# Kernel optimization log

Measured on AMD Instinct MI355X. Metric: run time of the kernel, lower is better.

The kernel has to match this reference:

```python
import jax, jax.numpy as jnp
import numpy as np

N_NODES = 100000
N_EDGES = 1200000
D_IN, D_HID, D_OUT = 64, 64, 16


def setup_inputs() -> dict:
    key = jax.random.key(0)
    ks = jax.random.split(key, 8)
    x = jax.random.normal(ks[0], (N_NODES, D_IN), dtype=jnp.float32)
    edge_index = jax.random.randint(ks[1], (2, N_EDGES), 0, N_NODES, dtype=jnp.int64)
    edge_weight = jax.random.uniform(ks[2], (N_EDGES,), dtype=jnp.float32)
    s1 = 1.0 / np.sqrt(D_IN)
    s2 = 1.0 / np.sqrt(D_HID)
    W1l = jax.random.normal(ks[3], (D_IN, D_HID), dtype=jnp.float32) * s1
    W1r = jax.random.normal(ks[4], (D_IN, D_HID), dtype=jnp.float32) * s1
    b1 = jnp.zeros((D_HID,), dtype=jnp.float32)
    W2l = jax.random.normal(ks[5], (D_HID, D_OUT), dtype=jnp.float32) * s2
    W2r = jax.random.normal(ks[6], (D_HID, D_OUT), dtype=jnp.float32) * s2
    b2 = jnp.zeros((D_OUT,), dtype=jnp.float32)
    return {"x": x, "edge_index": edge_index, "edge_weight": edge_weight,
            "W1l": W1l, "b1": b1, "W1r": W1r, "W2l": W2l, "b2": b2, "W2r": W2r}


def _sage_conv(x, src, dst, ew, Wl, bl, Wr):
    # message: x_j * w_e, mean-aggregated by in-degree count at dst (PyG SAGEConv aggr='mean')
    msg = x[src] * ew[:, None]                                  # [E, D]
    agg = jax.ops.segment_sum(msg, dst, num_segments=x.shape[0])
    cnt = jax.ops.segment_sum(jnp.ones_like(ew), dst, num_segments=x.shape[0])
    agg = agg / jnp.maximum(cnt, 1.0)[:, None]
    return agg @ Wl + bl + x @ Wr                               # lin_l(agg) + lin_r(x)


def reference(x, edge_index, edge_weight, W1l, b1, W1r, W2l, b2, W2r):
    # eval mode: dropout is identity
    src, dst = edge_index[0], edge_index[1]
    h = jax.nn.relu(_sage_conv(x, src, dst, edge_weight, W1l, b1, W1r))
    out = _sage_conv(h, src, dst, edge_weight, W2l, b2, W2r)
    return out
```

## Files before the change

kernel.cpp:

```cpp
#include <hip/hip_runtime.h>

#define N_NODES 100000
#define N_EDGES 1200000
#define NB_SCAN ((N_NODES + 1023) / 1024)

__global__ __launch_bounds__(256) void k_hist(const int* __restrict__ ei,
                                              int* __restrict__ deg) {
    int e = blockIdx.x * 256 + threadIdx.x;
    if (e < N_EDGES) atomicAdd(&deg[ei[N_EDGES + e]], 1);
}

__global__ __launch_bounds__(256) void k_scanA(const int* __restrict__ deg,
                                               int* __restrict__ bsum) {
    const int b = blockIdx.x, t = threadIdx.x;
    const int base = b * 1024 + t * 4;
    int s = 0;
    #pragma unroll
    for (int i = 0; i < 4; ++i) {
        int idx = base + i;
        if (idx < N_NODES) s += deg[idx];
    }
    #pragma unroll
    for (int off = 1; off < 64; off <<= 1) s += __shfl_xor(s, off);
    __shared__ int part[4];
    if ((t & 63) == 0) part[t >> 6] = s;
    __syncthreads();
    if (t == 0) bsum[b] = part[0] + part[1] + part[2] + part[3];
}

__global__ void k_scanB(const int* __restrict__ bsum, int* __restrict__ boff) {
    if (threadIdx.x == 0) {
        int acc = 0;
        for (int i = 0; i < NB_SCAN; ++i) { boff[i] = acc; acc += bsum[i]; }
    }
}

__global__ __launch_bounds__(256) void k_scanC(const int* __restrict__ deg,
                                               const int* __restrict__ boff,
                                               int* __restrict__ row_ptr) {
    __shared__ int tot[256];
    const int b = blockIdx.x, t = threadIdx.x;
    const int base = b * 1024 + t * 4;
    int d[4]; int s = 0;
    #pragma unroll
    for (int i = 0; i < 4; ++i) {
        int idx = base + i;
        d[i] = (idx < N_NODES) ? deg[idx] : 0;
        s += d[i];
    }
    tot[t] = s;
    __syncthreads();
    for (int off = 1; off < 256; off <<= 1) {
        int v = (t >= off) ? tot[t - off] : 0;
        __syncthreads();
        tot[t] += v;
        __syncthreads();
    }
    int run = boff[b] + tot[t] - s;
    #pragma unroll
    for (int i = 0; i < 4; ++i) {
        int idx = base + i;
        if (idx < N_NODES) { row_ptr[idx] = run; run += d[i]; }
    }
    if (b == 0 && t == 0) row_ptr[N_NODES] = N_EDGES;
}

__global__ __launch_bounds__(256) void k_fill(const int* __restrict__ ei,
                                              const float* __restrict__ ew,
                                              int* __restrict__ cursor,
                                              uint2* __restrict__ csr) {
    int e = blockIdx.x * 256 + threadIdx.x;
    if (e < N_EDGES) {
        int src = ei[e];
        int dst = ei[N_EDGES + e];
        int pos = atomicAdd(&cursor[dst], 1);
        csr[pos] = make_uint2((unsigned)src, __float_as_uint(ew[e]));
    }
}

__global__ __launch_bounds__(512, 2) void k_l1(const float* __restrict__ x,
                                               const int* __restrict__ row_ptr,
                                               const uint2* __restrict__ csr,
                                               const float* __restrict__ W1l,
                                               const float* __restrict__ b1,
                                               const float* __restrict__ W1r,
                                               const float* __restrict__ W2l,
                                               const float* __restrict__ W2r,
                                               float* __restrict__ z2,
                                               float* __restrict__ hw2r) {
    __shared__ float w1l[64 * 64];
    __shared__ float w1r[64 * 64];
    __shared__ float w2l[64 * 17];
    __shared__ float w2r[64 * 17];
    for (int i = threadIdx.x; i < 64 * 64; i += 512) { w1l[i] = W1l[i]; w1r[i] = W1r[i]; }
    for (int i = threadIdx.x; i < 64 * 16; i += 512) {
        int k = i >> 4, j = i & 15;
        w2l[k * 17 + j] = W2l[i];
        w2r[k * 17 + j] = W2r[i];
    }
    __syncthreads();
    const int lane = threadIdx.x & 63;
    const int wid  = blockIdx.x * 8 + (threadIdx.x >> 6);
    const int nw   = gridDim.x * 8;
    const int j = lane & 15, g = lane >> 4;
    const float b1v = b1[lane];
    for (int n = wid; n < N_NODES; n += nw) {
        const int r0 = row_ptr[n], r1 = row_ptr[n + 1];
        const int deg = r1 - r0;
        float acc0 = 0.f, acc1 = 0.f, acc2 = 0.f, acc3 = 0.f;
        for (int base = r0; base < r1; base += 64) {
            const int m = r1 - base < 64 ? r1 - base : 64;
            uint2 sw = make_uint2(0u, 0u);
            if (lane < m) sw = csr[base + lane];
            const int sv = (int)sw.x;
            const int wv = (int)sw.y;
            int it = 0;
            for (; it + 4 <= m; it += 4) {
                int s0 = __builtin_amdgcn_readlane(sv, it);
                int s1 = __builtin_amdgcn_readlane(sv, it + 1);
                int s2 = __builtin_amdgcn_readlane(sv, it + 2);
                int s3 = __builtin_amdgcn_readlane(sv, it + 3);
                float w0 = __int_as_float(__builtin_amdgcn_readlane(wv, it));
                float w1 = __int_as_float(__builtin_amdgcn_readlane(wv, it + 1));
                float w2 = __int_as_float(__builtin_amdgcn_readlane(wv, it + 2));
                float w3 = __int_as_float(__builtin_amdgcn_readlane(wv, it + 3));
                float v0 = x[(size_t)s0 * 64 + lane];
                float v1 = x[(size_t)s1 * 64 + lane];
                float v2 = x[(size_t)s2 * 64 + lane];
                float v3 = x[(size_t)s3 * 64 + lane];
                acc0 = fmaf(v0, w0, acc0);
                acc1 = fmaf(v1, w1, acc1);
                acc2 = fmaf(v2, w2, acc2);
                acc3 = fmaf(v3, w3, acc3);
            }
            for (; it < m; ++it) {
                int   s = __builtin_amdgcn_readlane(sv, it);
                float w = __int_as_float(__builtin_amdgcn_readlane(wv, it));
                acc0 = fmaf(x[(size_t)s * 64 + lane], w, acc0);
            }
        }
        const float acc = (acc0 + acc1) + (acc2 + acc3);
        const float inv = 1.f / (float)(deg > 0 ? deg : 1);
        const float av  = acc * inv;
        const float xr  = x[(size_t)n * 64 + lane];
        float hacc = b1v;
        #pragma unroll
        for (int k = 0; k < 64; ++k) {
            float ak = __shfl(av, k);
            float xk = __shfl(xr, k);
            hacc = fmaf(ak, w1l[k * 64 + lane], hacc);
            hacc = fmaf(xk, w1r[k * 64 + lane], hacc);
        }
        const float hval = hacc > 0.f ? hacc : 0.f;

        float azv = 0.f, arv = 0.f;
        #pragma unroll
        for (int i = 0; i < 16; ++i) {
            int   k  = g * 16 + i;
            float hk = __shfl(hval, k);
            azv = fmaf(hk, w2l[k * 17 + j], azv);
            arv = fmaf(hk, w2r[k * 17 + j], arv);
        }
        azv += __shfl_xor(azv, 16); azv += __shfl_xor(azv, 32);
        arv += __shfl_xor(arv, 16); arv += __shfl_xor(arv, 32);
        if (g == 0) {
            z2[(size_t)n * 16 + j]   = azv;
            hw2r[(size_t)n * 16 + j] = arv;
        }
    }
}

__global__ __launch_bounds__(256) void k_l2(const float* __restrict__ z2,
                                            const int* __restrict__ row_ptr,
                                            const uint2* __restrict__ csr,
                                            const float* __restrict__ b2,
                                            const float* __restrict__ hw2r,
                                            float* __restrict__ out) {
    const int lane = threadIdx.x & 63;
    const int wid  = blockIdx.x * 4 + (threadIdx.x >> 6);
    const int nw   = gridDim.x * 4;
    const int j = lane & 15, g = lane >> 4;
    for (int n = wid; n < N_NODES; n += nw) {
        const int r0 = row_ptr[n], r1 = row_ptr[n + 1];
        const int deg = r1 - r0;
        float a = 0.f;
        int i = r0 + g;
        for (; i + 4 < r1; i += 8) {
            uint2 e0 = csr[i];
            uint2 e1 = csr[i + 4];
            float z0 = z2[(size_t)e0.x * 16 + j];
            float z1 = z2[(size_t)e1.x * 16 + j];
            a = fmaf(z0, __uint_as_float(e0.y), a);
            a = fmaf(z1, __uint_as_float(e1.y), a);
        }
        if (i < r1) {
            uint2 e0 = csr[i];
            a = fmaf(z2[(size_t)e0.x * 16 + j], __uint_as_float(e0.y), a);
        }
        a += __shfl_xor(a, 16); a += __shfl_xor(a, 32);
        if (g == 0) {
            const float inv = 1.f / (float)(deg > 0 ? deg : 1);
            out[(size_t)n * 16 + j] = a * inv + b2[j] + hw2r[(size_t)n * 16 + j];
        }
    }
}

extern "C" void kernel_launch(void* const* d_in, const int* in_sizes, int n_in,
                              void* d_out, int out_size, void* d_ws, size_t ws_size,
                              hipStream_t stream) {
    const float* x   = (const float*)d_in[0];
    const int*   ei  = (const int*)d_in[1];
    const float* ew  = (const float*)d_in[2];
    const float* W1l = (const float*)d_in[3];
    const float* b1  = (const float*)d_in[4];
    const float* W1r = (const float*)d_in[5];
    const float* W2l = (const float*)d_in[6];
    const float* b2  = (const float*)d_in[7];
    const float* W2r = (const float*)d_in[8];
    float* out = (float*)d_out;

    char* w = (char*)d_ws;
    uint2* csr     = (uint2*)w;  w += (size_t)N_EDGES * 8;
    float* z2      = (float*)w;  w += (size_t)N_NODES * 16 * 4;
    float* hw2r    = (float*)w;  w += (size_t)N_NODES * 16 * 4;
    int*   deg     = (int*)w;    w += (size_t)N_NODES * 4;
    int*   row_ptr = (int*)w;    w += (size_t)(N_NODES + 1) * 4;
    int*   cursor  = (int*)w;    w += (size_t)N_NODES * 4;
    int*   bsum    = (int*)w;    w += 128 * 4;
    int*   boff    = (int*)w;

    hipMemsetAsync(deg, 0, (size_t)N_NODES * 4, stream);

    k_hist <<<(N_EDGES + 255) / 256, 256, 0, stream>>>(ei, deg);
    k_scanA<<<NB_SCAN, 256, 0, stream>>>(deg, bsum);
    k_scanB<<<1, 64, 0, stream>>>(bsum, boff);
    k_scanC<<<NB_SCAN, 256, 0, stream>>>(deg, boff, row_ptr);
    hipMemcpyAsync(cursor, row_ptr, (size_t)N_NODES * 4,
                   hipMemcpyDeviceToDevice, stream);
    k_fill <<<(N_EDGES + 255) / 256, 256, 0, stream>>>(ei, ew, cursor, csr);
    k_l1   <<<1024, 512, 0, stream>>>(x, row_ptr, csr, W1l, b1, W1r, W2l, W2r, z2, hw2r);
    k_l2   <<<1024, 256, 0, stream>>>(z2, row_ptr, csr, b2, hw2r, out);
}
```

Measured before the change: 530.8 us.

## Split layer-1 into gather and dense kernels, fuse cursor init, batch layer-2 loads

The fused layer-1 kernel is split into a lightweight gather kernel that writes the mean-aggregated features to a new workspace buffer and a separate dense kernel that does both matmuls. The gather kernel no longer needs the 36 KB of LDS weights, so more waves can stay resident to hide the latency of the random reads. The cost is an extra 25.6 MB round trip through global memory. The scan kernel now also writes the cursor array, which removes a device-to-device memcpy, and the layer-2 loop issues four clamped edge loads per iteration to expose more memory-level parallelism.

```diff
diff --git a/kernel.cpp b/kernel.cpp
--- a/kernel.cpp
+++ b/kernel.cpp
@@ -37,7 +37,8 @@
 
 __global__ __launch_bounds__(256) void k_scanC(const int* __restrict__ deg,
                                                const int* __restrict__ boff,
-                                               int* __restrict__ row_ptr) {
+                                               int* __restrict__ row_ptr,
+                                               int* __restrict__ cursor) {
     __shared__ int tot[256];
     const int b = blockIdx.x, t = threadIdx.x;
     const int base = b * 1024 + t * 4;
@@ -60,7 +61,7 @@
     #pragma unroll
     for (int i = 0; i < 4; ++i) {
         int idx = base + i;
-        if (idx < N_NODES) { row_ptr[idx] = run; run += d[i]; }
+        if (idx < N_NODES) { row_ptr[idx] = run; cursor[idx] = run; run += d[i]; }
     }
     if (b == 0 && t == 0) row_ptr[N_NODES] = N_EDGES;
 }
@@ -78,32 +79,13 @@
     }
 }
 
-__global__ __launch_bounds__(512, 2) void k_l1(const float* __restrict__ x,
-                                               const int* __restrict__ row_ptr,
-                                               const uint2* __restrict__ csr,
-                                               const float* __restrict__ W1l,
-                                               const float* __restrict__ b1,
-                                               const float* __restrict__ W1r,
-                                               const float* __restrict__ W2l,
-                                               const float* __restrict__ W2r,
-                                               float* __restrict__ z2,
-                                               float* __restrict__ hw2r) {
-    __shared__ float w1l[64 * 64];
-    __shared__ float w1r[64 * 64];
-    __shared__ float w2l[64 * 17];
-    __shared__ float w2r[64 * 17];
-    for (int i = threadIdx.x; i < 64 * 64; i += 512) { w1l[i] = W1l[i]; w1r[i] = W1r[i]; }
-    for (int i = threadIdx.x; i < 64 * 16; i += 512) {
-        int k = i >> 4, j = i & 15;
-        w2l[k * 17 + j] = W2l[i];
-        w2r[k * 17 + j] = W2r[i];
-    }
-    __syncthreads();
+__global__ __launch_bounds__(256) void k_gather(const float* __restrict__ x,
+                                                const int* __restrict__ row_ptr,
+                                                const uint2* __restrict__ csr,
+                                                float* __restrict__ av) {
     const int lane = threadIdx.x & 63;
-    const int wid  = blockIdx.x * 8 + (threadIdx.x >> 6);
-    const int nw   = gridDim.x * 8;
-    const int j = lane & 15, g = lane >> 4;
-    const float b1v = b1[lane];
+    const int wid  = blockIdx.x * 4 + (threadIdx.x >> 6);
+    const int nw   = gridDim.x * 4;
     for (int n = wid; n < N_NODES; n += nw) {
         const int r0 = row_ptr[n], r1 = row_ptr[n + 1];
         const int deg = r1 - r0;
@@ -141,12 +123,42 @@
         }
         const float acc = (acc0 + acc1) + (acc2 + acc3);
         const float inv = 1.f / (float)(deg > 0 ? deg : 1);
-        const float av  = acc * inv;
+        av[(size_t)n * 64 + lane] = acc * inv;
+    }
+}
+
+__global__ __launch_bounds__(512) void k_node(const float* __restrict__ x,
+                                              const float* __restrict__ av,
+                                              const float* __restrict__ W1l,
+                                              const float* __restrict__ b1,
+                                              const float* __restrict__ W1r,
+                                              const float* __restrict__ W2l,
+                                              const float* __restrict__ W2r,
+                                              float* __restrict__ z2,
+                                              float* __restrict__ hw2r) {
+    __shared__ float w1l[64 * 64];
+    __shared__ float w1r[64 * 64];
+    __shared__ float w2l[64 * 17];
+    __shared__ float w2r[64 * 17];
+    for (int i = threadIdx.x; i < 64 * 64; i += 512) { w1l[i] = W1l[i]; w1r[i] = W1r[i]; }
+    for (int i = threadIdx.x; i < 64 * 16; i += 512) {
+        int k = i >> 4, j = i & 15;
+        w2l[k * 17 + j] = W2l[i];
+        w2r[k * 17 + j] = W2r[i];
+    }
+    __syncthreads();
+    const int lane = threadIdx.x & 63;
+    const int wid  = blockIdx.x * 8 + (threadIdx.x >> 6);
+    const int nw   = gridDim.x * 8;
+    const int j = lane & 15, g = lane >> 4;
+    const float b1v = b1[lane];
+    for (int n = wid; n < N_NODES; n += nw) {
+        const float avv = av[(size_t)n * 64 + lane];
         const float xr  = x[(size_t)n * 64 + lane];
         float hacc = b1v;
         #pragma unroll
         for (int k = 0; k < 64; ++k) {
-            float ak = __shfl(av, k);
+            float ak = __shfl(avv, k);
             float xk = __shfl(xr, k);
             hacc = fmaf(ak, w1l[k * 64 + lane], hacc);
             hacc = fmaf(xk, w1r[k * 64 + lane], hacc);
@@ -183,19 +195,23 @@
     for (int n = wid; n < N_NODES; n += nw) {
         const int r0 = row_ptr[n], r1 = row_ptr[n + 1];
         const int deg = r1 - r0;
+        const int rmax = r1 - 1;
         float a = 0.f;
-        int i = r0 + g;
-        for (; i + 4 < r1; i += 8) {
-            uint2 e0 = csr[i];
-            uint2 e1 = csr[i + 4];
-            float z0 = z2[(size_t)e0.x * 16 + j];
-            float z1 = z2[(size_t)e1.x * 16 + j];
-            a = fmaf(z0, __uint_as_float(e0.y), a);
-            a = fmaf(z1, __uint_as_float(e1.y), a);
-        }
-        if (i < r1) {
-            uint2 e0 = csr[i];
-            a = fmaf(z2[(size_t)e0.x * 16 + j], __uint_as_float(e0.y), a);
+        for (int i0 = r0 + g; i0 < r1; i0 += 16) {
+            uint2 e[4]; float wt[4];
+            #pragma unroll
+            for (int u = 0; u < 4; ++u) {
+                int idx = i0 + u * 4;
+                int idc = idx < rmax ? idx : rmax;
+                e[u]  = csr[idc];
+                wt[u] = (idx < r1) ? __uint_as_float(e[u].y) : 0.f;
+            }
+            float zv[4];
+            #pragma unroll
+            for (int u = 0; u < 4; ++u)
+                zv[u] = z2[(size_t)e[u].x * 16 + j];
+            #pragma unroll
+            for (int u = 0; u < 4; ++u) a = fmaf(zv[u], wt[u], a);
         }
         a += __shfl_xor(a, 16); a += __shfl_xor(a, 32);
         if (g == 0) {
@@ -221,6 +237,7 @@
 
     char* w = (char*)d_ws;
     uint2* csr     = (uint2*)w;  w += (size_t)N_EDGES * 8;
+    float* av      = (float*)w;  w += (size_t)N_NODES * 64 * 4;
     float* z2      = (float*)w;  w += (size_t)N_NODES * 16 * 4;
     float* hw2r    = (float*)w;  w += (size_t)N_NODES * 16 * 4;
     int*   deg     = (int*)w;    w += (size_t)N_NODES * 4;
@@ -231,13 +248,12 @@
 
     hipMemsetAsync(deg, 0, (size_t)N_NODES * 4, stream);
 
-    k_hist <<<(N_EDGES + 255) / 256, 256, 0, stream>>>(ei, deg);
-    k_scanA<<<NB_SCAN, 256, 0, stream>>>(deg, bsum);
-    k_scanB<<<1, 64, 0, stream>>>(bsum, boff);
-    k_scanC<<<NB_SCAN, 256, 0, stream>>>(deg, boff, row_ptr);
-    hipMemcpyAsync(cursor, row_ptr, (size_t)N_NODES * 4,
-                   hipMemcpyDeviceToDevice, stream);
-    k_fill <<<(N_EDGES + 255) / 256, 256, 0, stream>>>(ei, ew, cursor, csr);
-    k_l1   <<<1024, 512, 0, stream>>>(x, row_ptr, csr, W1l, b1, W1r, W2l, W2r, z2, hw2r);
-    k_l2   <<<1024, 256, 0, stream>>>(z2, row_ptr, csr, b2, hw2r, out);
-}
+    k_hist  <<<(N_EDGES + 255) / 256, 256, 0, stream>>>(ei, deg);
+    k_scanA <<<NB_SCAN, 256, 0, stream>>>(deg, bsum);
+    k_scanB <<<1, 64, 0, stream>>>(bsum, boff);
+    k_scanC <<<NB_SCAN, 256, 0, stream>>>(deg, boff, row_ptr, cursor);
+    k_fill  <<<(N_EDGES + 255) / 256, 256, 0, stream>>>(ei, ew, cursor, csr);
+    k_gather<<<2048, 256, 0, stream>>>(x, row_ptr, csr, av);
+    k_node  <<<1024, 512, 0, stream>>>(x, av, W1l, b1, W1r, W2l, W2r, z2, hw2r);
+    k_l2    <<<1024, 256, 0, stream>>>(z2, row_ptr, csr, b2, hw2r, out);
+}
```

Measured after the change: 485.5 us. -8.5%, faster.
